# Optimization experiments

Hardware: AMD Instinct MI355X
Metric: run time of the kernel (lower is better)

## Reference

```python
import jax, jax.numpy as jnp
import numpy as np

N_NODES = 100000
N_EDGES = 1200000
D_FEAT = 64


def setup_inputs() -> dict:
    key = jax.random.key(0)
    k1, k2, k3 = jax.random.split(key, 3)
    x = jax.random.normal(k1, (N_NODES, D_FEAT), dtype=jnp.float32)
    edge_index = jax.random.randint(k2, (2, N_EDGES), 0, N_NODES, dtype=jnp.int64)
    edge_weight = jax.random.uniform(k3, (N_EDGES, 1), dtype=jnp.float32)
    return {"x": x, "edge_index": edge_index, "edge_weight": edge_weight}


def reference(x, edge_index, edge_weight):
    # flow = source_to_target: j = edge_index[0] (source), i = edge_index[1] (target)
    src, dst = edge_index[0], edge_index[1]
    # message: x_j  (gather along node_dim=-2)
    msg = x[src]                       # [E, D]
    # aggregate: scatter-'sum' with edge_weight scaling
    msg = msg * edge_weight            # [E, D]
    out = jax.ops.segment_sum(msg, dst, num_segments=N_NODES)  # [N, D]
    # update: identity
    return out
```

## Files before the change

kernel.cpp:

```cpp
#include <hip/hip_runtime.h>
#include <hip/hip_bf16.h>


constexpr int D_FEAT        = 64;
constexpr int BIN_SHIFT     = 7;
constexpr int NODES_PER_BIN = 1 << BIN_SHIFT;
constexpr int NBINS_MAX     = 1024;
constexpr int BIN_CAP       = 2048;
constexpr int EPB           = 4096;
constexpr int OVF_CAP       = 32768;

__device__ __forceinline__ int wave_incl_scan(int v, int lane) {
    #pragma unroll
    for (int d = 1; d < 64; d <<= 1) {
        int t = __shfl_up(v, d);
        if (lane >= d) v += t;
    }
    return v;
}

__device__ __forceinline__ unsigned short f32_to_bf16_rn(float f) {
    unsigned int u = __float_as_uint(f);
    u += 0x7FFFu + ((u >> 16) & 1u);
    return (unsigned short)(u >> 16);
}

__global__ __launch_bounds__(1024) void mp_partition(
    const int* __restrict__ src, const int* __restrict__ dst,
    const float* __restrict__ w, const float* __restrict__ x,
    ushort* __restrict__ xb, int n4,
    int*  __restrict__ gcnt,
    int2* __restrict__ payload,
    int*  __restrict__ ovf_cnt, int4* __restrict__ ovf,
    int n_edges, int nbins)
{
    __shared__ int cnt[NBINS_MAX];
    __shared__ int start[NBINS_MAX];
    __shared__ int cur[NBINS_MAX];
    __shared__ int gbase[NBINS_MAX];
    __shared__ unsigned short binof[EPB];
    __shared__ int2 sorted[EPB];
    __shared__ int wsum[16];

    const int t    = threadIdx.x;
    const int lane = t & 63;
    const int wid  = t >> 6;
    const int base = blockIdx.x * EPB;
    const int nblk = min(EPB, n_edges - base);

    for (int i = blockIdx.x * 1024 + t; i < n4; i += gridDim.x * 1024) {
        const float4 v = reinterpret_cast<const float4*>(x)[i];
        ushort4 o;
        o.x = f32_to_bf16_rn(v.x);
        o.y = f32_to_bf16_rn(v.y);
        o.z = f32_to_bf16_rn(v.z);
        o.w = f32_to_bf16_rn(v.w);
        reinterpret_cast<ushort4*>(xb)[i] = o;
    }

    if (t < NBINS_MAX) cnt[t] = 0;
    __syncthreads();

    const int i4 = (base >> 2) + t;
    int4 d4 = make_int4(0, 0, 0, 0);
    bool have = (i4 * 4 < n_edges);
    if (have) {
        d4 = reinterpret_cast<const int4*>(dst)[i4];
        atomicAdd(&cnt[d4.x >> BIN_SHIFT], 1);
        atomicAdd(&cnt[d4.y >> BIN_SHIFT], 1);
        atomicAdd(&cnt[d4.z >> BIN_SHIFT], 1);
        atomicAdd(&cnt[d4.w >> BIN_SHIFT], 1);
    }
    __syncthreads();

    const int c = (t < nbins) ? cnt[t] : 0;
    const int incl = wave_incl_scan(c, lane);
    if (lane == 63) wsum[wid] = incl;
    __syncthreads();
    int woff = 0;
    #pragma unroll
    for (int k = 0; k < 16; ++k) woff += (k < wid) ? wsum[k] : 0;
    const int excl = woff + incl - c;
    if (t < nbins) {
        start[t] = excl;
        cur[t]   = excl;
        if (c > 0) gbase[t] = atomicAdd(&gcnt[t], c);
    }
    __syncthreads();

    if (have) {
        const int4   s4 = reinterpret_cast<const int4*>(src)[i4];
        const float4 w4 = reinterpret_cast<const float4*>(w)[i4];
        const int   dd[4] = {d4.x, d4.y, d4.z, d4.w};
        const int   ss[4] = {s4.x, s4.y, s4.z, s4.w};
        const float ww[4] = {w4.x, w4.y, w4.z, w4.w};
        #pragma unroll
        for (int j = 0; j < 4; ++j) {
            const int b   = dd[j] >> BIN_SHIFT;
            const int low = dd[j] & (NODES_PER_BIN - 1);
            const int p   = atomicAdd(&cur[b], 1);
            sorted[p] = make_int2((low << 20) | ss[j], __float_as_int(ww[j]));
            binof[p]  = (unsigned short)b;
        }
    }
    __syncthreads();

    #pragma unroll
    for (int k = 0; k < EPB / 1024; ++k) {
        const int i = k * 1024 + t;
        if (i >= nblk) break;
        const int b    = binof[i];
        const int idx  = i - start[b];
        const int gpos = gbase[b] + idx;
        const int2 e   = sorted[i];
        if (gpos < BIN_CAP) {
            payload[(size_t)b * BIN_CAP + gpos] = e;
        } else {
            const int op = atomicAdd(ovf_cnt, 1);
            if (op < OVF_CAP)
                ovf[op] = make_int4((b << BIN_SHIFT) + (e.x >> 20),
                                    e.x & 0xFFFFF, e.y, 0);
        }
    }
}

__global__ __launch_bounds__(512) void mp_bin_gather(
    const ushort* __restrict__ xb,
    const float*  __restrict__ x,
    const int*  __restrict__ gcnt,
    const int2* __restrict__ payload,
    const int*  __restrict__ ovf_cnt, const int4* __restrict__ ovf,
    float* __restrict__ out, int n_nodes)
{
    __shared__ int2 sraw[BIN_CAP];
    __shared__ int2 sedge[BIN_CAP];
    __shared__ int ncnt[NODES_PER_BIN];
    __shared__ int nstart[NODES_PER_BIN + 1];
    __shared__ int ncur[NODES_PER_BIN];

    const int b    = blockIdx.x;
    const int t    = threadIdx.x;
    const int lane = t & 63;
    const int wid  = t >> 6;
    const int sub  = lane >> 3;
    const int fq   = lane & 7;
    const int fg   = fq * 8;

    const int m = min(gcnt[b], BIN_CAP);
    const int2* pl = payload + (size_t)b * BIN_CAP;

    for (int i = t; i < NODES_PER_BIN; i += 512) ncnt[i] = 0;
    __syncthreads();

    for (int i = t; i < m; i += 512) {
        const int2 e = pl[i];
        sraw[i] = e;
        atomicAdd(&ncnt[e.x >> 20], 1);
    }
    __syncthreads();

    if (t < 64) {
        const int a0 = ncnt[t], a1 = ncnt[64 + t];
        const int s0 = wave_incl_scan(a0, t);
        const int s1 = wave_incl_scan(a1, t);
        const int tot0 = __shfl(s0, 63);
        nstart[t]      = s0 - a0;
        nstart[64 + t] = tot0 + s1 - a1;
        if (t == 63) nstart[128] = tot0 + s1;
    }
    __syncthreads();
    for (int i = t; i < NODES_PER_BIN; i += 512) ncur[i] = nstart[i];
    __syncthreads();

    for (int i = t; i < m; i += 512) {
        const int2 e = sraw[i];
        const int p  = atomicAdd(&ncur[e.x >> 20], 1);
        sedge[p] = e;
    }
    __syncthreads();

    const int novf = *ovf_cnt;

    #pragma unroll
    for (int nb = 0; nb < 16; nb += 8) {
        const int n    = wid * 16 + nb + sub;
        const int node = (b << BIN_SHIFT) + n;
        const int s0 = nstart[n];
        const int s1 = nstart[n + 1];

        float a0 = 0.f, a1 = 0.f, a2 = 0.f, a3 = 0.f;
        float a4 = 0.f, a5 = 0.f, a6 = 0.f, a7 = 0.f;

        int e = s0;
        for (; e + 2 <= s1; e += 2) {
            const int2 pA = sedge[e];
            const int2 pB = sedge[e + 1];
            const uint4 xA = *reinterpret_cast<const uint4*>(
                xb + (size_t)(pA.x & 0xFFFFF) * D_FEAT + fg);
            const uint4 xB = *reinterpret_cast<const uint4*>(
                xb + (size_t)(pB.x & 0xFFFFF) * D_FEAT + fg);
            const float wA = __int_as_float(pA.y);
            const float wB = __int_as_float(pB.y);
            a0 = fmaf(__uint_as_float(xA.x << 16),         wA, a0);
            a1 = fmaf(__uint_as_float(xA.x & 0xFFFF0000u), wA, a1);
            a2 = fmaf(__uint_as_float(xA.y << 16),         wA, a2);
            a3 = fmaf(__uint_as_float(xA.y & 0xFFFF0000u), wA, a3);
            a4 = fmaf(__uint_as_float(xA.z << 16),         wA, a4);
            a5 = fmaf(__uint_as_float(xA.z & 0xFFFF0000u), wA, a5);
            a6 = fmaf(__uint_as_float(xA.w << 16),         wA, a6);
            a7 = fmaf(__uint_as_float(xA.w & 0xFFFF0000u), wA, a7);
            a0 = fmaf(__uint_as_float(xB.x << 16),         wB, a0);
            a1 = fmaf(__uint_as_float(xB.x & 0xFFFF0000u), wB, a1);
            a2 = fmaf(__uint_as_float(xB.y << 16),         wB, a2);
            a3 = fmaf(__uint_as_float(xB.y & 0xFFFF0000u), wB, a3);
            a4 = fmaf(__uint_as_float(xB.z << 16),         wB, a4);
            a5 = fmaf(__uint_as_float(xB.z & 0xFFFF0000u), wB, a5);
            a6 = fmaf(__uint_as_float(xB.w << 16),         wB, a6);
            a7 = fmaf(__uint_as_float(xB.w & 0xFFFF0000u), wB, a7);
        }
        if (e < s1) {
            const int2 p = sedge[e];
            const uint4 xv = *reinterpret_cast<const uint4*>(
                xb + (size_t)(p.x & 0xFFFFF) * D_FEAT + fg);
            const float ww = __int_as_float(p.y);
            a0 = fmaf(__uint_as_float(xv.x << 16),         ww, a0);
            a1 = fmaf(__uint_as_float(xv.x & 0xFFFF0000u), ww, a1);
            a2 = fmaf(__uint_as_float(xv.y << 16),         ww, a2);
            a3 = fmaf(__uint_as_float(xv.y & 0xFFFF0000u), ww, a3);
            a4 = fmaf(__uint_as_float(xv.z << 16),         ww, a4);
            a5 = fmaf(__uint_as_float(xv.z & 0xFFFF0000u), ww, a5);
            a6 = fmaf(__uint_as_float(xv.w << 16),         ww, a6);
            a7 = fmaf(__uint_as_float(xv.w & 0xFFFF0000u), ww, a7);
        }

        if (node < n_nodes) {
            if (novf > 0) {
                const int lim = min(novf, OVF_CAP);
                for (int j = 0; j < lim; ++j) {
                    const int4 o = ovf[j];
                    if (o.x == node) {
                        const float* xr = x + (size_t)o.y * D_FEAT + fg;
                        const float ww = __int_as_float(o.z);
                        a0 = fmaf(xr[0], ww, a0); a1 = fmaf(xr[1], ww, a1);
                        a2 = fmaf(xr[2], ww, a2); a3 = fmaf(xr[3], ww, a3);
                        a4 = fmaf(xr[4], ww, a4); a5 = fmaf(xr[5], ww, a5);
                        a6 = fmaf(xr[6], ww, a6); a7 = fmaf(xr[7], ww, a7);
                    }
                }
            }
            float* orow = out + (size_t)node * D_FEAT + fg;
            *reinterpret_cast<float4*>(orow)     = make_float4(a0, a1, a2, a3);
            *reinterpret_cast<float4*>(orow + 4) = make_float4(a4, a5, a6, a7);
        }
    }
}

__global__ __launch_bounds__(256) void mp_scatter_atomic(
    const float* __restrict__ x, const int* __restrict__ src,
    const int* __restrict__ dst, const float* __restrict__ w,
    float* __restrict__ out, int n_edges)
{
    const int gtid = blockIdx.x * blockDim.x + threadIdx.x;
    const int edge = gtid >> 6;
    const int lane = threadIdx.x & 63;
    if (edge >= n_edges) return;
    const int s = src[edge];
    const int d = dst[edge];
    const float ww = w[edge];
    atomicAdd(&out[(size_t)d * D_FEAT + lane], x[(size_t)s * D_FEAT + lane] * ww);
}

extern "C" void kernel_launch(void* const* d_in, const int* in_sizes, int n_in,
                              void* d_out, int out_size, void* d_ws, size_t ws_size,
                              hipStream_t stream)
{
    const float* x          = (const float*)d_in[0];
    const int*   edge_index = (const int*)d_in[1];
    const float* w          = (const float*)d_in[2];
    float*       out        = (float*)d_out;

    const int n_edges = in_sizes[1] / 2;
    const int n_nodes = in_sizes[0] / D_FEAT;
    const int* src = edge_index;
    const int* dst = edge_index + n_edges;

    const int nbins = (n_nodes + NODES_PER_BIN - 1) >> BIN_SHIFT;

    int*    gcnt    = (int*)d_ws;
    int*    ovf_cnt = gcnt + NBINS_MAX;
    int4*   ovf     = (int4*)(gcnt + NBINS_MAX + 64);
    int2*   payload = (int2*)(ovf + OVF_CAP);
    ushort* xb      = (ushort*)(payload + (size_t)nbins * BIN_CAP);
    const size_t need = (size_t)(NBINS_MAX + 64) * 4 + (size_t)OVF_CAP * 16
                      + (size_t)nbins * BIN_CAP * 8
                      + (size_t)n_nodes * D_FEAT * 2;

    const bool ok = (ws_size >= need) && (nbins <= NBINS_MAX) && ((n_edges & 3) == 0)
                 && ((n_nodes * D_FEAT) % 4 == 0);

    if (ok) {
        hipMemsetAsync(gcnt, 0, (size_t)(NBINS_MAX + 64) * 4, stream);
        const int n4 = n_nodes * D_FEAT / 4;
        const int g1 = (n_edges + EPB - 1) / EPB;
        mp_partition<<<g1, 1024, 0, stream>>>(src, dst, w, x, xb, n4,
                                              gcnt, payload, ovf_cnt, ovf,
                                              n_edges, nbins);
        mp_bin_gather<<<nbins, 512, 0, stream>>>(xb, x, gcnt, payload,
                                                 ovf_cnt, ovf, out, n_nodes);
        return;
    }

    hipMemsetAsync(d_out, 0, (size_t)out_size * sizeof(float), stream);
    const int grid = (int)(((size_t)n_edges * 64 + 255) / 256);
    mp_scatter_atomic<<<grid, 256, 0, stream>>>(x, src, dst, w, out, n_edges);
}
```

Baseline: 123.8 us.

## Halve bin size to 64 nodes and unroll the gather loop by four

```diff
diff --git a/kernel.cpp b/kernel.cpp
--- a/kernel.cpp
+++ b/kernel.cpp
@@ -3,10 +3,10 @@
 
 
 constexpr int D_FEAT        = 64;
-constexpr int BIN_SHIFT     = 7;
+constexpr int BIN_SHIFT     = 6;
 constexpr int NODES_PER_BIN = 1 << BIN_SHIFT;
-constexpr int NBINS_MAX     = 1024;
-constexpr int BIN_CAP       = 2048;
+constexpr int NBINS_MAX     = 2048;
+constexpr int BIN_CAP       = 1024;
 constexpr int EPB           = 4096;
 constexpr int OVF_CAP       = 32768;
 
@@ -58,7 +58,8 @@
         reinterpret_cast<ushort4*>(xb)[i] = o;
     }
 
-    if (t < NBINS_MAX) cnt[t] = 0;
+    cnt[t] = 0;
+    cnt[t + 1024] = 0;
     __syncthreads();
 
     const int i4 = (base >> 2) + t;
@@ -73,18 +74,26 @@
     }
     __syncthreads();
 
-    const int c = (t < nbins) ? cnt[t] : 0;
-    const int incl = wave_incl_scan(c, lane);
+    const int b2 = t * 2;
+    const int c0 = (b2     < nbins) ? cnt[b2]     : 0;
+    const int c1 = (b2 + 1 < nbins) ? cnt[b2 + 1] : 0;
+    const int l  = c0 + c1;
+    const int incl = wave_incl_scan(l, lane);
     if (lane == 63) wsum[wid] = incl;
     __syncthreads();
     int woff = 0;
     #pragma unroll
     for (int k = 0; k < 16; ++k) woff += (k < wid) ? wsum[k] : 0;
-    const int excl = woff + incl - c;
-    if (t < nbins) {
-        start[t] = excl;
-        cur[t]   = excl;
-        if (c > 0) gbase[t] = atomicAdd(&gcnt[t], c);
+    const int excl = woff + incl - l;
+    if (b2 < nbins) {
+        start[b2] = excl;
+        cur[b2]   = excl;
+        if (c0 > 0) gbase[b2] = atomicAdd(&gcnt[b2], c0);
+    }
+    if (b2 + 1 < nbins) {
+        start[b2 + 1] = excl + c0;
+        cur[b2 + 1]   = excl + c0;
+        if (c1 > 0) gbase[b2 + 1] = atomicAdd(&gcnt[b2 + 1], c1);
     }
     __syncthreads();
 
@@ -149,7 +158,7 @@
     const int m = min(gcnt[b], BIN_CAP);
     const int2* pl = payload + (size_t)b * BIN_CAP;
 
-    for (int i = t; i < NODES_PER_BIN; i += 512) ncnt[i] = 0;
+    if (t < NODES_PER_BIN) ncnt[t] = 0;
     __syncthreads();
 
     for (int i = t; i < m; i += 512) {
@@ -160,16 +169,13 @@
     __syncthreads();
 
     if (t < 64) {
-        const int a0 = ncnt[t], a1 = ncnt[64 + t];
+        const int a0 = ncnt[t];
         const int s0 = wave_incl_scan(a0, t);
-        const int s1 = wave_incl_scan(a1, t);
-        const int tot0 = __shfl(s0, 63);
-        nstart[t]      = s0 - a0;
-        nstart[64 + t] = tot0 + s1 - a1;
-        if (t == 63) nstart[128] = tot0 + s1;
-    }
-    __syncthreads();
-    for (int i = t; i < NODES_PER_BIN; i += 512) ncur[i] = nstart[i];
+        nstart[t] = s0 - a0;
+        if (t == 63) nstart[64] = s0;
+    }
+    __syncthreads();
+    if (t < NODES_PER_BIN) ncur[t] = nstart[t];
     __syncthreads();
 
     for (int i = t; i < m; i += 512) {
@@ -181,77 +187,124 @@
 
     const int novf = *ovf_cnt;
 
-    #pragma unroll
-    for (int nb = 0; nb < 16; nb += 8) {
-        const int n    = wid * 16 + nb + sub;
-        const int node = (b << BIN_SHIFT) + n;
-        const int s0 = nstart[n];
-        const int s1 = nstart[n + 1];
-
-        float a0 = 0.f, a1 = 0.f, a2 = 0.f, a3 = 0.f;
-        float a4 = 0.f, a5 = 0.f, a6 = 0.f, a7 = 0.f;
-
-        int e = s0;
-        for (; e + 2 <= s1; e += 2) {
-            const int2 pA = sedge[e];
-            const int2 pB = sedge[e + 1];
-            const uint4 xA = *reinterpret_cast<const uint4*>(
-                xb + (size_t)(pA.x & 0xFFFFF) * D_FEAT + fg);
-            const uint4 xB = *reinterpret_cast<const uint4*>(
-                xb + (size_t)(pB.x & 0xFFFFF) * D_FEAT + fg);
-            const float wA = __int_as_float(pA.y);
-            const float wB = __int_as_float(pB.y);
-            a0 = fmaf(__uint_as_float(xA.x << 16),         wA, a0);
-            a1 = fmaf(__uint_as_float(xA.x & 0xFFFF0000u), wA, a1);
-            a2 = fmaf(__uint_as_float(xA.y << 16),         wA, a2);
-            a3 = fmaf(__uint_as_float(xA.y & 0xFFFF0000u), wA, a3);
-            a4 = fmaf(__uint_as_float(xA.z << 16),         wA, a4);
-            a5 = fmaf(__uint_as_float(xA.z & 0xFFFF0000u), wA, a5);
-            a6 = fmaf(__uint_as_float(xA.w << 16),         wA, a6);
-            a7 = fmaf(__uint_as_float(xA.w & 0xFFFF0000u), wA, a7);
-            a0 = fmaf(__uint_as_float(xB.x << 16),         wB, a0);
-            a1 = fmaf(__uint_as_float(xB.x & 0xFFFF0000u), wB, a1);
-            a2 = fmaf(__uint_as_float(xB.y << 16),         wB, a2);
-            a3 = fmaf(__uint_as_float(xB.y & 0xFFFF0000u), wB, a3);
-            a4 = fmaf(__uint_as_float(xB.z << 16),         wB, a4);
-            a5 = fmaf(__uint_as_float(xB.z & 0xFFFF0000u), wB, a5);
-            a6 = fmaf(__uint_as_float(xB.w << 16),         wB, a6);
-            a7 = fmaf(__uint_as_float(xB.w & 0xFFFF0000u), wB, a7);
-        }
-        if (e < s1) {
-            const int2 p = sedge[e];
-            const uint4 xv = *reinterpret_cast<const uint4*>(
-                xb + (size_t)(p.x & 0xFFFFF) * D_FEAT + fg);
-            const float ww = __int_as_float(p.y);
-            a0 = fmaf(__uint_as_float(xv.x << 16),         ww, a0);
-            a1 = fmaf(__uint_as_float(xv.x & 0xFFFF0000u), ww, a1);
-            a2 = fmaf(__uint_as_float(xv.y << 16),         ww, a2);
-            a3 = fmaf(__uint_as_float(xv.y & 0xFFFF0000u), ww, a3);
-            a4 = fmaf(__uint_as_float(xv.z << 16),         ww, a4);
-            a5 = fmaf(__uint_as_float(xv.z & 0xFFFF0000u), ww, a5);
-            a6 = fmaf(__uint_as_float(xv.w << 16),         ww, a6);
-            a7 = fmaf(__uint_as_float(xv.w & 0xFFFF0000u), ww, a7);
-        }
-
-        if (node < n_nodes) {
-            if (novf > 0) {
-                const int lim = min(novf, OVF_CAP);
-                for (int j = 0; j < lim; ++j) {
-                    const int4 o = ovf[j];
-                    if (o.x == node) {
-                        const float* xr = x + (size_t)o.y * D_FEAT + fg;
-                        const float ww = __int_as_float(o.z);
-                        a0 = fmaf(xr[0], ww, a0); a1 = fmaf(xr[1], ww, a1);
-                        a2 = fmaf(xr[2], ww, a2); a3 = fmaf(xr[3], ww, a3);
-                        a4 = fmaf(xr[4], ww, a4); a5 = fmaf(xr[5], ww, a5);
-                        a6 = fmaf(xr[6], ww, a6); a7 = fmaf(xr[7], ww, a7);
-                    }
+    const int n    = wid * 8 + sub;
+    const int node = (b << BIN_SHIFT) + n;
+    const int s0 = nstart[n];
+    const int s1 = nstart[n + 1];
+
+    float a0 = 0.f, a1 = 0.f, a2 = 0.f, a3 = 0.f;
+    float a4 = 0.f, a5 = 0.f, a6 = 0.f, a7 = 0.f;
+
+    int e = s0;
+    for (; e + 4 <= s1; e += 4) {
+        const int2 p0 = sedge[e];
+        const int2 p1 = sedge[e + 1];
+        const int2 p2 = sedge[e + 2];
+        const int2 p3 = sedge[e + 3];
+        const uint4 x0 = *reinterpret_cast<const uint4*>(
+            xb + (size_t)(p0.x & 0xFFFFF) * D_FEAT + fg);
+        const uint4 x1 = *reinterpret_cast<const uint4*>(
+            xb + (size_t)(p1.x & 0xFFFFF) * D_FEAT + fg);
+        const uint4 x2 = *reinterpret_cast<const uint4*>(
+            xb + (size_t)(p2.x & 0xFFFFF) * D_FEAT + fg);
+        const uint4 x3 = *reinterpret_cast<const uint4*>(
+            xb + (size_t)(p3.x & 0xFFFFF) * D_FEAT + fg);
+        const float w0 = __int_as_float(p0.y);
+        const float w1 = __int_as_float(p1.y);
+        const float w2 = __int_as_float(p2.y);
+        const float w3 = __int_as_float(p3.y);
+        a0 = fmaf(__uint_as_float(x0.x << 16),         w0, a0);
+        a1 = fmaf(__uint_as_float(x0.x & 0xFFFF0000u), w0, a1);
+        a2 = fmaf(__uint_as_float(x0.y << 16),         w0, a2);
+        a3 = fmaf(__uint_as_float(x0.y & 0xFFFF0000u), w0, a3);
+        a4 = fmaf(__uint_as_float(x0.z << 16),         w0, a4);
+        a5 = fmaf(__uint_as_float(x0.z & 0xFFFF0000u), w0, a5);
+        a6 = fmaf(__uint_as_float(x0.w << 16),         w0, a6);
+        a7 = fmaf(__uint_as_float(x0.w & 0xFFFF0000u), w0, a7);
+        a0 = fmaf(__uint_as_float(x1.x << 16),         w1, a0);
+        a1 = fmaf(__uint_as_float(x1.x & 0xFFFF0000u), w1, a1);
+        a2 = fmaf(__uint_as_float(x1.y << 16),         w1, a2);
+        a3 = fmaf(__uint_as_float(x1.y & 0xFFFF0000u), w1, a3);
+        a4 = fmaf(__uint_as_float(x1.z << 16),         w1, a4);
+        a5 = fmaf(__uint_as_float(x1.z & 0xFFFF0000u), w1, a5);
+        a6 = fmaf(__uint_as_float(x1.w << 16),         w1, a6);
+        a7 = fmaf(__uint_as_float(x1.w & 0xFFFF0000u), w1, a7);
+        a0 = fmaf(__uint_as_float(x2.x << 16),         w2, a0);
+        a1 = fmaf(__uint_as_float(x2.x & 0xFFFF0000u), w2, a1);
+        a2 = fmaf(__uint_as_float(x2.y << 16),         w2, a2);
+        a3 = fmaf(__uint_as_float(x2.y & 0xFFFF0000u), w2, a3);
+        a4 = fmaf(__uint_as_float(x2.z << 16),         w2, a4);
+        a5 = fmaf(__uint_as_float(x2.z & 0xFFFF0000u), w2, a5);
+        a6 = fmaf(__uint_as_float(x2.w << 16),         w2, a6);
+        a7 = fmaf(__uint_as_float(x2.w & 0xFFFF0000u), w2, a7);
+        a0 = fmaf(__uint_as_float(x3.x << 16),         w3, a0);
+        a1 = fmaf(__uint_as_float(x3.x & 0xFFFF0000u), w3, a1);
+        a2 = fmaf(__uint_as_float(x3.y << 16),         w3, a2);
+        a3 = fmaf(__uint_as_float(x3.y & 0xFFFF0000u), w3, a3);
+        a4 = fmaf(__uint_as_float(x3.z << 16),         w3, a4);
+        a5 = fmaf(__uint_as_float(x3.z & 0xFFFF0000u), w3, a5);
+        a6 = fmaf(__uint_as_float(x3.w << 16),         w3, a6);
+        a7 = fmaf(__uint_as_float(x3.w & 0xFFFF0000u), w3, a7);
+    }
+    for (; e + 2 <= s1; e += 2) {
+        const int2 p0 = sedge[e];
+        const int2 p1 = sedge[e + 1];
+        const uint4 x0 = *reinterpret_cast<const uint4*>(
+            xb + (size_t)(p0.x & 0xFFFFF) * D_FEAT + fg);
+        const uint4 x1 = *reinterpret_cast<const uint4*>(
+            xb + (size_t)(p1.x & 0xFFFFF) * D_FEAT + fg);
+        const float w0 = __int_as_float(p0.y);
+        const float w1 = __int_as_float(p1.y);
+        a0 = fmaf(__uint_as_float(x0.x << 16),         w0, a0);
+        a1 = fmaf(__uint_as_float(x0.x & 0xFFFF0000u), w0, a1);
+        a2 = fmaf(__uint_as_float(x0.y << 16),         w0, a2);
+        a3 = fmaf(__uint_as_float(x0.y & 0xFFFF0000u), w0, a3);
+        a4 = fmaf(__uint_as_float(x0.z << 16),         w0, a4);
+        a5 = fmaf(__uint_as_float(x0.z & 0xFFFF0000u), w0, a5);
+        a6 = fmaf(__uint_as_float(x0.w << 16),         w0, a6);
+        a7 = fmaf(__uint_as_float(x0.w & 0xFFFF0000u), w0, a7);
+        a0 = fmaf(__uint_as_float(x1.x << 16),         w1, a0);
+        a1 = fmaf(__uint_as_float(x1.x & 0xFFFF0000u), w1, a1);
+        a2 = fmaf(__uint_as_float(x1.y << 16),         w1, a2);
+        a3 = fmaf(__uint_as_float(x1.y & 0xFFFF0000u), w1, a3);
+        a4 = fmaf(__uint_as_float(x1.z << 16),         w1, a4);
+        a5 = fmaf(__uint_as_float(x1.z & 0xFFFF0000u), w1, a5);
+        a6 = fmaf(__uint_as_float(x1.w << 16),         w1, a6);
+        a7 = fmaf(__uint_as_float(x1.w & 0xFFFF0000u), w1, a7);
+    }
+    if (e < s1) {
+        const int2 p = sedge[e];
+        const uint4 xv = *reinterpret_cast<const uint4*>(
+            xb + (size_t)(p.x & 0xFFFFF) * D_FEAT + fg);
+        const float ww = __int_as_float(p.y);
+        a0 = fmaf(__uint_as_float(xv.x << 16),         ww, a0);
+        a1 = fmaf(__uint_as_float(xv.x & 0xFFFF0000u), ww, a1);
+        a2 = fmaf(__uint_as_float(xv.y << 16),         ww, a2);
+        a3 = fmaf(__uint_as_float(xv.y & 0xFFFF0000u), ww, a3);
+        a4 = fmaf(__uint_as_float(xv.z << 16),         ww, a4);
+        a5 = fmaf(__uint_as_float(xv.z & 0xFFFF0000u), ww, a5);
+        a6 = fmaf(__uint_as_float(xv.w << 16),         ww, a6);
+        a7 = fmaf(__uint_as_float(xv.w & 0xFFFF0000u), ww, a7);
+    }
+
+    if (node < n_nodes) {
+        if (novf > 0) {
+            const int lim = min(novf, OVF_CAP);
+            for (int j = 0; j < lim; ++j) {
+                const int4 o = ovf[j];
+                if (o.x == node) {
+                    const float* xr = x + (size_t)o.y * D_FEAT + fg;
+                    const float ww = __int_as_float(o.z);
+                    a0 = fmaf(xr[0], ww, a0); a1 = fmaf(xr[1], ww, a1);
+                    a2 = fmaf(xr[2], ww, a2); a3 = fmaf(xr[3], ww, a3);
+                    a4 = fmaf(xr[4], ww, a4); a5 = fmaf(xr[5], ww, a5);
+                    a6 = fmaf(xr[6], ww, a6); a7 = fmaf(xr[7], ww, a7);
                 }
             }
-            float* orow = out + (size_t)node * D_FEAT + fg;
-            *reinterpret_cast<float4*>(orow)     = make_float4(a0, a1, a2, a3);
-            *reinterpret_cast<float4*>(orow + 4) = make_float4(a4, a5, a6, a7);
         }
+        float* orow = out + (size_t)node * D_FEAT + fg;
+        *reinterpret_cast<float4*>(orow)     = make_float4(a0, a1, a2, a3);
+        *reinterpret_cast<float4*>(orow + 4) = make_float4(a4, a5, a6, a7);
     }
 }
 
```

Measured after the change: 127.8 us. 1.03x slower.
